# Kernel tuning notes

Measured on AMD Instinct MI355X. Metric: run time of the kernel, lower is better.

Reference implementation:

```python
import jax, jax.numpy as jnp
import numpy as np

B, C, D, O = 262144, 256, 64, 8


def setup_inputs() -> dict:
    key = jax.random.key(0)
    k1, k2, k3, k4 = jax.random.split(key, 4)
    inputs = jax.random.normal(k1, (B, D), dtype=jnp.float32)
    cluster_centers = jax.random.normal(k2, (C, D), dtype=jnp.float32)
    # widths initialized ~ N(1.0, 0.05) as in the layer
    widths = 1.0 + 0.05 * jax.random.normal(k3, (C,), dtype=jnp.float32)
    # rule_weights ~ N(0, 0.05)
    rule_weights = 0.05 * jax.random.normal(k4, (C, O), dtype=jnp.float32)
    return {"inputs": inputs, "cluster_centers": cluster_centers,
            "widths": widths, "rule_weights": rule_weights}


def reference(inputs, cluster_centers, widths, rule_weights):
    # Squared L2 distances via ||a-c||^2 = ||a||^2 + ||c||^2 - 2 a.c
    # (avoids materializing the [B, C, D] broadcast diff tensor)
    x_sq = jnp.sum(inputs * inputs, axis=1, keepdims=True)          # [B, 1]
    c_sq = jnp.sum(cluster_centers * cluster_centers, axis=1)       # [C]
    cross = inputs @ cluster_centers.T                               # [B, C]
    dists_squared = x_sq + c_sq[None, :] - 2.0 * cross               # [B, C]
    # Gaussian membership with per-cluster widths
    memb = jnp.exp(-dists_squared / (2.0 * widths * widths))         # [B, C]
    # Normalize over clusters (sum-normalization, not softmax-of-logits)
    memb_norm = memb / jnp.sum(memb, axis=1, keepdims=True)          # [B, C]
    # Weighted rule consequents
    return memb_norm @ rule_weights                                  # [B, O]
```

## Files before the change

### kernel.cpp

```cpp
#include <hip/hip_runtime.h>


#define NB 262144
#define NC 256
#define ND 64
#define NO 8

typedef __attribute__((ext_vector_type(8))) short short8;
typedef __attribute__((ext_vector_type(8))) _Float16 half8;
typedef __attribute__((ext_vector_type(16))) float floatx16;

#define WOFF 20480
#define WS_SHORTS 28672
#define WS_UINT4 3584

__device__ __host__ inline unsigned short f2bf(float f) {
    unsigned u = __builtin_bit_cast(unsigned, f);
    u = u + 0x7FFFu + ((u >> 16) & 1u);
    return (unsigned short)(u >> 16);
}
__device__ inline unsigned short f2h(float f) {
    return __builtin_bit_cast(unsigned short, (_Float16)f);
}

__global__ void fuzzy_prep(const float* __restrict__ centers,
                           const float* __restrict__ widths,
                           const float* __restrict__ W,
                           unsigned short* __restrict__ ws) {
    const int lane = threadIdx.x;
    const int col = lane & 31;
    const int h = lane >> 5;

    if (blockIdx.x < 8) {
        const int t = blockIdx.x;
        const int c = 32 * t + ((col & 19) | ((col & 4) << 1) | ((col & 8) >> 1));
        const float* cr = centers + c * ND;
        float w = widths[c];
        float kk = 1.4426950408889634f / (2.0f * w * w);

        float vv[4][8];
        float part = 0.0f;
#pragma unroll
        for (int kd = 0; kd < 4; ++kd) {
            const float4* p = (const float4*)(cr + kd * 16 + h * 8);
            float4 a0 = p[0], a1 = p[1];
            vv[kd][0] = a0.x; vv[kd][1] = a0.y; vv[kd][2] = a0.z; vv[kd][3] = a0.w;
            vv[kd][4] = a1.x; vv[kd][5] = a1.y; vv[kd][6] = a1.z; vv[kd][7] = a1.w;
#pragma unroll
            for (int j = 0; j < 8; ++j) part = fmaf(vv[kd][j], vv[kd][j], part);
        }
        float csq = part + __shfl_xor(part, 32, 64);

#pragma unroll
        for (int kd = 0; kd < 4; ++kd)
#pragma unroll
            for (int j = 0; j < 8; ++j)
                ws[((t * 5 + kd) * 64 + lane) * 8 + j] = f2h(2.0f * kk * vv[kd][j]);

        unsigned short v[8] = {0, 0, 0, 0, 0, 0, 0, 0};
        if (h == 0) {
            float kh = (float)(_Float16)kk;
            float kl = kk - kh;
            float Bc = csq * kk;
            float Bh = (float)(_Float16)Bc;
            float Bl = Bc - Bh;
            v[0] = f2h(-kh);
            v[1] = f2h(-kh);
            v[2] = f2h(-kl);
            v[3] = f2h(-Bh);
            v[4] = f2h(-Bl);
        }
#pragma unroll
        for (int j = 0; j < 8; ++j)
            ws[((t * 5 + 4) * 64 + lane) * 8 + j] = v[j];
    } else {
        const int k2base = (blockIdx.x - 8) * 4;
#pragma unroll
        for (int kq = 0; kq < 4; ++kq) {
            int k2 = k2base + kq;
#pragma unroll
            for (int j = 0; j < 8; ++j) {
                int c = k2 * 16 + h * 8 + j;
                float val = (col < NO) ? W[c * NO + col] : (col == 8 ? 1.0f : 0.0f);
                ws[WOFF + (k2 * 64 + lane) * 8 + j] = f2bf(val);
            }
        }
    }
}

__global__ __launch_bounds__(512, 4) void fuzzy_main(
    const float* __restrict__ x,
    const uint4* __restrict__ ws4,
    float* __restrict__ out) {
    __shared__ short lds_s[WS_SHORTS];

    const int tid = threadIdx.x;
    const int wave = tid >> 6;
    const int lane = tid & 63;
    const int col = lane & 31;
    const int h = lane >> 5;
    const int bbase = (blockIdx.x * 8 + wave) * 64;

    {
        uint4* l4 = (uint4*)lds_s;
#pragma unroll
        for (int i = 0; i < 7; ++i) l4[tid + i * 512] = ws4[tid + i * 512];
    }

    half8 xh[2][4];
    half8 f12[2];
#pragma unroll
    for (int u = 0; u < 2; ++u) {
        const float* xrow = x + (size_t)(bbase + u * 32 + col) * ND;
        float part = 0.0f;
#pragma unroll
        for (int kd = 0; kd < 4; ++kd) {
            const float4* p = (const float4*)(xrow + kd * 16 + h * 8);
            float4 v0 = p[0], v1 = p[1];
            float v[8] = {v0.x, v0.y, v0.z, v0.w, v1.x, v1.y, v1.z, v1.w};
            half8 hh;
#pragma unroll
            for (int j = 0; j < 8; ++j) {
                part = fmaf(v[j], v[j], part);
                hh[j] = (_Float16)v[j];
            }
            xh[u][kd] = hh;
        }
        float xsq = part + __shfl_xor(part, 32, 64);
        float sh = (float)(_Float16)xsq;
        float sl = xsq - sh;
        half8 f;
#pragma unroll
        for (int j = 0; j < 8; ++j) f[j] = (_Float16)0.0f;
        if (h == 0) {
            f[0] = (_Float16)sh;
            f[1] = (_Float16)sl;
            f[2] = (_Float16)sh;
            f[3] = (_Float16)1.0f;
            f[4] = (_Float16)1.0f;
        }
        f12[u] = f;
    }

    __syncthreads();

    floatx16 acc2[2];
#pragma unroll
    for (int u = 0; u < 2; ++u)
#pragma unroll
        for (int i = 0; i < 16; ++i) acc2[u][i] = 0.0f;

#pragma unroll 2
    for (int t = 0; t < 8; ++t) {
        const half8 A0 = *(const half8*)&lds_s[((t * 5 + 0) * 64 + lane) * 8];
        const half8 A1 = *(const half8*)&lds_s[((t * 5 + 1) * 64 + lane) * 8];
        const half8 A2 = *(const half8*)&lds_s[((t * 5 + 2) * 64 + lane) * 8];
        const half8 A3 = *(const half8*)&lds_s[((t * 5 + 3) * 64 + lane) * 8];
        const half8 C12 = *(const half8*)&lds_s[((t * 5 + 4) * 64 + lane) * 8];
        const short8 w0 = *(const short8*)&lds_s[WOFF + ((2 * t + 0) * 64 + lane) * 8];
        const short8 w1 = *(const short8*)&lds_s[WOFF + ((2 * t + 1) * 64 + lane) * 8];

#pragma unroll
        for (int u = 0; u < 2; ++u) {
            floatx16 acc;
#pragma unroll
            for (int i = 0; i < 16; ++i) acc[i] = 0.0f;
            acc = __builtin_amdgcn_mfma_f32_32x32x16_f16(A0, xh[u][0], acc, 0, 0, 0);
            acc = __builtin_amdgcn_mfma_f32_32x32x16_f16(A1, xh[u][1], acc, 0, 0, 0);
            acc = __builtin_amdgcn_mfma_f32_32x32x16_f16(A2, xh[u][2], acc, 0, 0, 0);
            acc = __builtin_amdgcn_mfma_f32_32x32x16_f16(A3, xh[u][3], acc, 0, 0, 0);
            acc = __builtin_amdgcn_mfma_f32_32x32x16_f16(C12, f12[u], acc, 0, 0, 0);

            unsigned p0 = __builtin_bit_cast(unsigned, __builtin_amdgcn_exp2f(acc[0]));
            unsigned p1 = __builtin_bit_cast(unsigned, __builtin_amdgcn_exp2f(acc[1]));
            unsigned p2 = __builtin_bit_cast(unsigned, __builtin_amdgcn_exp2f(acc[2]));
            unsigned p3 = __builtin_bit_cast(unsigned, __builtin_amdgcn_exp2f(acc[3]));
            unsigned p4 = __builtin_bit_cast(unsigned, __builtin_amdgcn_exp2f(acc[4]));
            unsigned p5 = __builtin_bit_cast(unsigned, __builtin_amdgcn_exp2f(acc[5]));
            unsigned p6 = __builtin_bit_cast(unsigned, __builtin_amdgcn_exp2f(acc[6]));
            unsigned p7 = __builtin_bit_cast(unsigned, __builtin_amdgcn_exp2f(acc[7]));
            unsigned p8 = __builtin_bit_cast(unsigned, __builtin_amdgcn_exp2f(acc[8]));
            unsigned p9 = __builtin_bit_cast(unsigned, __builtin_amdgcn_exp2f(acc[9]));
            unsigned pa = __builtin_bit_cast(unsigned, __builtin_amdgcn_exp2f(acc[10]));
            unsigned pb = __builtin_bit_cast(unsigned, __builtin_amdgcn_exp2f(acc[11]));
            unsigned pc = __builtin_bit_cast(unsigned, __builtin_amdgcn_exp2f(acc[12]));
            unsigned pd = __builtin_bit_cast(unsigned, __builtin_amdgcn_exp2f(acc[13]));
            unsigned pe = __builtin_bit_cast(unsigned, __builtin_amdgcn_exp2f(acc[14]));
            unsigned pf = __builtin_bit_cast(unsigned, __builtin_amdgcn_exp2f(acc[15]));
            uint4 q0, q1;
            q0.x = __builtin_amdgcn_perm(p1, p0, 0x07060302u);
            q0.y = __builtin_amdgcn_perm(p3, p2, 0x07060302u);
            q0.z = __builtin_amdgcn_perm(p5, p4, 0x07060302u);
            q0.w = __builtin_amdgcn_perm(p7, p6, 0x07060302u);
            q1.x = __builtin_amdgcn_perm(p9, p8, 0x07060302u);
            q1.y = __builtin_amdgcn_perm(pb, pa, 0x07060302u);
            q1.z = __builtin_amdgcn_perm(pd, pc, 0x07060302u);
            q1.w = __builtin_amdgcn_perm(pf, pe, 0x07060302u);
            short8 pf0 = __builtin_bit_cast(short8, q0);
            short8 pf1 = __builtin_bit_cast(short8, q1);

            acc2[u] = __builtin_amdgcn_mfma_f32_32x32x16_bf16(w0, pf0, acc2[u], 0, 0, 0);
            acc2[u] = __builtin_amdgcn_mfma_f32_32x32x16_bf16(w1, pf1, acc2[u], 0, 0, 0);
        }
    }

#pragma unroll
    for (int u = 0; u < 2; ++u) {
        float S = acc2[u][4];
        float Sp = __shfl_xor(S, 32, 64);
        if (h) S = Sp;
        float inv = 1.0f / S;
        float4 r;
        r.x = acc2[u][0] * inv;
        r.y = acc2[u][1] * inv;
        r.z = acc2[u][2] * inv;
        r.w = acc2[u][3] * inv;
        ((float4*)(out + (size_t)(bbase + u * 32 + col) * NO))[h] = r;
    }
}

extern "C" void kernel_launch(void* const* d_in, const int* in_sizes, int n_in,
                              void* d_out, int out_size, void* d_ws, size_t ws_size,
                              hipStream_t stream) {
    const float* x       = (const float*)d_in[0];
    const float* centers = (const float*)d_in[1];
    const float* widths  = (const float*)d_in[2];
    const float* W       = (const float*)d_in[3];
    float* out = (float*)d_out;
    unsigned short* ws = (unsigned short*)d_ws;

    fuzzy_prep<<<12, 64, 0, stream>>>(centers, widths, W, ws);
    fuzzy_main<<<NB / 512, 512, 0, stream>>>(x, (const uint4*)ws, out);
}
```

Before: 111.6 us.

## Fuse prep kernel into main kernel, computing LDS tables per block

Removes the separate prep launch and global workspace. Each block's waves build the scaled fp16 center fragments, bias terms and bf16 rule-weight fragments directly into shared memory. Input rows are prefetched into registers before this setup so their load latency overlaps the table construction. This trades a launch plus a global round trip for redundant per-block prep work and extra register pressure.

```diff
diff --git a/kernel.cpp b/kernel.cpp
--- a/kernel.cpp
+++ b/kernel.cpp
@@ -12,32 +12,43 @@
 
 #define WOFF 20480
 #define WS_SHORTS 28672
-#define WS_UINT4 3584
-
-__device__ __host__ inline unsigned short f2bf(float f) {
+
+__device__ inline unsigned short f2bf(float f) {
     unsigned u = __builtin_bit_cast(unsigned, f);
     u = u + 0x7FFFu + ((u >> 16) & 1u);
     return (unsigned short)(u >> 16);
 }
-__device__ inline unsigned short f2h(float f) {
-    return __builtin_bit_cast(unsigned short, (_Float16)f);
-}
-
-__global__ void fuzzy_prep(const float* __restrict__ centers,
-                           const float* __restrict__ widths,
-                           const float* __restrict__ W,
-                           unsigned short* __restrict__ ws) {
-    const int lane = threadIdx.x;
+
+__global__ __launch_bounds__(512, 4) void fuzzy_main(
+    const float* __restrict__ x,
+    const float* __restrict__ centers,
+    const float* __restrict__ widths,
+    const float* __restrict__ W,
+    float* __restrict__ out) {
+    __shared__ short lds_s[WS_SHORTS];
+
+    const int tid = threadIdx.x;
+    const int wave = tid >> 6;
+    const int lane = tid & 63;
     const int col = lane & 31;
     const int h = lane >> 5;
-
-    if (blockIdx.x < 8) {
-        const int t = blockIdx.x;
+    const int bbase = (blockIdx.x * 8 + wave) * 64;
+
+    float4 xr[2][8];
+#pragma unroll
+    for (int u = 0; u < 2; ++u) {
+        const float4* xp = (const float4*)(x + (size_t)(bbase + u * 32 + col) * ND);
+#pragma unroll
+        for (int kd = 0; kd < 4; ++kd) {
+            xr[u][2 * kd + 0] = xp[4 * kd + 2 * h + 0];
+            xr[u][2 * kd + 1] = xp[4 * kd + 2 * h + 1];
+        }
+    }
+
+    {
+        const int t = wave;
         const int c = 32 * t + ((col & 19) | ((col & 4) << 1) | ((col & 8) >> 1));
         const float* cr = centers + c * ND;
-        float w = widths[c];
-        float kk = 1.4426950408889634f / (2.0f * w * w);
-
         float vv[4][8];
         float part = 0.0f;
 #pragma unroll
@@ -50,73 +61,55 @@
             for (int j = 0; j < 8; ++j) part = fmaf(vv[kd][j], vv[kd][j], part);
         }
         float csq = part + __shfl_xor(part, 32, 64);
-
-#pragma unroll
-        for (int kd = 0; kd < 4; ++kd)
-#pragma unroll
-            for (int j = 0; j < 8; ++j)
-                ws[((t * 5 + kd) * 64 + lane) * 8 + j] = f2h(2.0f * kk * vv[kd][j]);
-
-        unsigned short v[8] = {0, 0, 0, 0, 0, 0, 0, 0};
+        float w = widths[c];
+        float kk = 1.4426950408889634f / (2.0f * w * w);
+
+#pragma unroll
+        for (int kd = 0; kd < 4; ++kd) {
+            half8 ah;
+#pragma unroll
+            for (int j = 0; j < 8; ++j) ah[j] = (_Float16)(2.0f * kk * vv[kd][j]);
+            *(half8*)&lds_s[((t * 5 + kd) * 64 + lane) * 8] = ah;
+        }
+        half8 av;
+#pragma unroll
+        for (int j = 0; j < 8; ++j) av[j] = (_Float16)0.0f;
         if (h == 0) {
             float kh = (float)(_Float16)kk;
             float kl = kk - kh;
             float Bc = csq * kk;
             float Bh = (float)(_Float16)Bc;
             float Bl = Bc - Bh;
-            v[0] = f2h(-kh);
-            v[1] = f2h(-kh);
-            v[2] = f2h(-kl);
-            v[3] = f2h(-Bh);
-            v[4] = f2h(-Bl);
-        }
-#pragma unroll
-        for (int j = 0; j < 8; ++j)
-            ws[((t * 5 + 4) * 64 + lane) * 8 + j] = v[j];
-    } else {
-        const int k2base = (blockIdx.x - 8) * 4;
-#pragma unroll
-        for (int kq = 0; kq < 4; ++kq) {
-            int k2 = k2base + kq;
+            av[0] = (_Float16)(-kh);
+            av[1] = (_Float16)(-kh);
+            av[2] = (_Float16)(-kl);
+            av[3] = (_Float16)(-Bh);
+            av[4] = (_Float16)(-Bl);
+        }
+        *(half8*)&lds_s[((t * 5 + 4) * 64 + lane) * 8] = av;
+
+#pragma unroll
+        for (int q = 0; q < 2; ++q) {
+            int k2 = 2 * t + q;
+            short8 wf;
 #pragma unroll
             for (int j = 0; j < 8; ++j) {
-                int c = k2 * 16 + h * 8 + j;
-                float val = (col < NO) ? W[c * NO + col] : (col == 8 ? 1.0f : 0.0f);
-                ws[WOFF + (k2 * 64 + lane) * 8 + j] = f2bf(val);
+                int c2 = k2 * 16 + h * 8 + j;
+                float val = (col < NO) ? W[c2 * NO + col] : (col == 8 ? 1.0f : 0.0f);
+                wf[j] = (short)f2bf(val);
             }
-        }
-    }
-}
-
-__global__ __launch_bounds__(512, 4) void fuzzy_main(
-    const float* __restrict__ x,
-    const uint4* __restrict__ ws4,
-    float* __restrict__ out) {
-    __shared__ short lds_s[WS_SHORTS];
-
-    const int tid = threadIdx.x;
-    const int wave = tid >> 6;
-    const int lane = tid & 63;
-    const int col = lane & 31;
-    const int h = lane >> 5;
-    const int bbase = (blockIdx.x * 8 + wave) * 64;
-
-    {
-        uint4* l4 = (uint4*)lds_s;
-#pragma unroll
-        for (int i = 0; i < 7; ++i) l4[tid + i * 512] = ws4[tid + i * 512];
+            *(short8*)&lds_s[WOFF + (k2 * 64 + lane) * 8] = wf;
+        }
     }
 
     half8 xh[2][4];
     half8 f12[2];
 #pragma unroll
     for (int u = 0; u < 2; ++u) {
-        const float* xrow = x + (size_t)(bbase + u * 32 + col) * ND;
         float part = 0.0f;
 #pragma unroll
         for (int kd = 0; kd < 4; ++kd) {
-            const float4* p = (const float4*)(xrow + kd * 16 + h * 8);
-            float4 v0 = p[0], v1 = p[1];
+            float4 v0 = xr[u][2 * kd], v1 = xr[u][2 * kd + 1];
             float v[8] = {v0.x, v0.y, v0.z, v0.w, v1.x, v1.y, v1.z, v1.w};
             half8 hh;
 #pragma unroll
@@ -227,8 +220,7 @@
     const float* widths  = (const float*)d_in[2];
     const float* W       = (const float*)d_in[3];
     float* out = (float*)d_out;
-    unsigned short* ws = (unsigned short*)d_ws;
-
-    fuzzy_prep<<<12, 64, 0, stream>>>(centers, widths, W, ws);
-    fuzzy_main<<<NB / 512, 512, 0, stream>>>(x, (const uint4*)ws, out);
+    (void)d_ws; (void)ws_size;
+
+    fuzzy_main<<<NB / 512, 512, 0, stream>>>(x, centers, widths, W, out);
 }
```

New measurement: 113.4 us. No clear change (+1.7%).
